# Performance work log

Measured on AMD Instinct MI355X. Metric: run time of the kernel, lower is better.

Reference implementation:

```python
import jax, jax.numpy as jnp
import numpy as np

B, T, WARM, H, FIN, MLPW = 8192, 30, 24, 128, 8, 128
WX = ['clouds','pres','precip','temp','rh','ghi','wind_x','wind_y']
TL = ['hour_sin','hour_cos','year_sin','year_cos','elev_angle','azimuth_sin','azimuth_cos']


def setup_inputs() -> dict:
    key = jax.random.key(0)
    ks = jax.random.split(key, 32)
    d = {}
    for i, n in enumerate(WX + TL):
        d[n] = jax.random.normal(ks[i], (B, T), dtype=jnp.float32)
    d['irradiance_in'] = jax.random.uniform(ks[20], (B, WARM), dtype=jnp.float32)
    s = lambda fan: 1.0 / np.sqrt(fan).astype(np.float32)
    # LSTM params (flax OptimizedLSTMCell math: fused input/hidden kernels, one bias), gate order i,f,g,o
    d['Wi'] = jax.random.normal(ks[21], (FIN, 4 * H), dtype=jnp.float32) * s(FIN)
    d['Wh'] = jax.random.normal(ks[22], (H, 4 * H), dtype=jnp.float32) * s(H)
    d['b'] = jnp.zeros((4 * H,), jnp.float32)
    # output head: MLP(depth=2, width=128) with relu, then Dense(1)
    d['W1'] = jax.random.normal(ks[23], (H, MLPW), dtype=jnp.float32) * s(H)
    d['b1'] = jnp.zeros((MLPW,), jnp.float32)
    d['W2'] = jax.random.normal(ks[24], (MLPW, MLPW), dtype=jnp.float32) * s(MLPW)
    d['b2'] = jnp.zeros((MLPW,), jnp.float32)
    d['Wout'] = jax.random.normal(ks[25], (MLPW, 1), dtype=jnp.float32) * s(MLPW)
    d['bout'] = jnp.zeros((1,), jnp.float32)
    return d


def reference(clouds, pres, precip, temp, rh, ghi, wind_x, wind_y,
              hour_sin, hour_cos, year_sin, year_cos, elev_angle, azimuth_sin, azimuth_cos,
              irradiance_in, Wi, Wh, b, W1, b1, W2, b2, Wout, bout):
    # FLAGS.weather=False path: x is the time/location feature stack [B, T, 7].
    # Weather features are accepted (as in the original dict) but unused.
    x = jnp.stack([hour_sin, hour_cos, year_sin, year_cos, elev_angle, azimuth_sin, azimuth_cos], axis=-1)
    warm_in = jnp.concatenate([x[:, :WARM], irradiance_in[..., None]], axis=-1)  # [B, 24, 8]
    auto_in = x[:, WARM:]                                                        # [B, 6, 7]

    def lstm_step(c, h, inp):
        z = inp @ Wi + h @ Wh + b                    # [B, 4H]
        i, f, g, o = jnp.split(z, 4, axis=-1)
        c2 = jax.nn.sigmoid(f) * c + jax.nn.sigmoid(i) * jnp.tanh(g)
        h2 = jax.nn.sigmoid(o) * jnp.tanh(c2)
        return c2, h2

    def out_mlp(h):
        h = jax.nn.relu(h @ W1 + b1)
        h = jax.nn.relu(h @ W2 + b2)
        return h @ Wout + bout                       # [..., 1]

    c0 = jnp.zeros((x.shape[0], H), x.dtype)
    h0 = jnp.zeros((x.shape[0], H), x.dtype)

    # warmup: teacher-forced LSTM over observed irradiance
    def warm_step(carry, xt):
        c, h = carry
        c, h = lstm_step(c, h, xt)
        return (c, h), h
    (c, h), hs = jax.lax.scan(warm_step, (c0, h0), jnp.swapaxes(warm_in, 0, 1))
    preds_warm = out_mlp(jnp.swapaxes(hs, 0, 1))     # [B, 24, 1]
    last_pred = preds_warm[:, -1]                    # [B, 1]

    def auto_step(carry, xt):
        c, h, p = carry
        c, h = lstm_step(c, h, jnp.concatenate([xt, p], axis=-1))
        p = out_mlp(h)
        return (c, h, p), p
    _, preds_auto = jax.lax.scan(auto_step, (c, h, last_pred), jnp.swapaxes(auto_in, 0, 1))
    preds_auto = jnp.swapaxes(preds_auto, 0, 1)      # [B, 6, 1]

    pred = jnp.concatenate([preds_warm, preds_auto], axis=1)  # [B, 30, 1]
    return jnp.squeeze(pred, axis=2)                 # [B, 30]
```

## Files before the change

### kernel.cpp

```cpp
#include <hip/hip_runtime.h>


#define T_STEPS 30
#define WARM_N  24

typedef _Float16 h8 __attribute__((ext_vector_type(8)));
typedef __attribute__((ext_vector_type(4))) float float4v;

struct FeatPtrs { const float* f[7]; };

#if __has_builtin(__builtin_amdgcn_rcpf)
#define RCP(x) __builtin_amdgcn_rcpf(x)
#else
#define RCP(x) (1.0f/(x))
#endif

__device__ __forceinline__ float sigm(float x){ return RCP(1.0f + __expf(-x)); }
__device__ __forceinline__ float tanh_(float x){ return 1.0f - 2.0f*RCP(1.0f + __expf(2.0f*x)); }

__global__ void pack_weights(const float* __restrict__ Wi, const float* __restrict__ Wh,
                             const float* __restrict__ W1, const float* __restrict__ W2,
                             _Float16* __restrict__ ws)
{
  int idx = blockIdx.x * 256 + threadIdx.x;
  if (idx >= 224 * 512) return;
  int f    = idx >> 9;
  int r    = idx & 511;
  int lane = r >> 3, j = r & 7;
  int kk   = ((lane >> 4) << 3) + j;
  int c16  = lane & 15;
  float v = 0.0f;
  if (f < 160){
    int wt = f / 20, rem = f % 20, g = rem / 5, ks = rem % 5;
    int col = g * 128 + wt * 16 + c16;
    if (ks == 0) v = (kk < 8) ? Wi[kk * 512 + col] : 0.0f;
    else         v = Wh[((ks - 1) * 32 + kk) * 512 + col];
  } else {
    int f2 = f - 160;
    const float* W = (f2 < 32) ? W1 : W2;
    int f3 = f2 & 31;
    int wt = f3 >> 2, ks = f3 & 3;
    v = W[(ks * 32 + kk) * 128 + wt * 16 + c16];
  }
  ws[idx] = (_Float16)v;
}

#define MFMA16 __builtin_amdgcn_mfma_f32_16x16x32_f16

#define INIT_ACC(ACC) \
  _Pragma("unroll") for (int g_ = 0; g_ < 4; ++g_) \
    _Pragma("unroll") for (int r_ = 0; r_ < 4; ++r_) ACC[g_][r_] = bzv[g_];

#define INIT4(V, B) \
  _Pragma("unroll") for (int r_ = 0; r_ < 4; ++r_) V[r_] = (B);

#define ZA(ACC, M1V, XBUF, HOFF, DO1) \
  { h8 ax_ = *(const h8*)&xp[XBUF][(HOFF) + aoff]; \
    _Pragma("unroll") for (int g_ = 0; g_ < 4; ++g_) \
      ACC[g_] = MFMA16(ax_, Bz[g_][0], ACC[g_], 0, 0, 0); } \
  _Pragma("unroll") for (int ks_ = 0; ks_ < 4; ++ks_){ \
    h8 ah_ = *(const h8*)&hp[ks_ * 1280 + (HOFF) + aoff]; \
    _Pragma("unroll") for (int g_ = 0; g_ < 4; ++g_) \
      ACC[g_] = MFMA16(ah_, Bz[g_][1 + ks_], ACC[g_], 0, 0, 0); \
    if (DO1) M1V = MFMA16(ah_, B1f[ks_], M1V, 0, 0, 0); }

#define WRITE_O1(M1V, HOFF) \
  _Pragma("unroll") for (int r_ = 0; r_ < 4; ++r_) \
    o1p[wb + (HOFF) + (kq * 4 + r_) * 40] = (_Float16)fmaxf(M1V[r_], 0.0f);

#define GATES(ACC, CB, HOFF) \
  _Pragma("unroll") for (int r_ = 0; r_ < 4; ++r_){ \
    float zi_ = ACC[0][r_], zf_ = ACC[1][r_], zg_ = ACC[2][r_], zo_ = ACC[3][r_]; \
    float c2_ = sigm(zf_) * cst[(CB) + r_] + sigm(zi_) * tanh_(zg_); \
    cst[(CB) + r_] = c2_; \
    float h2_ = sigm(zo_) * tanh_(c2_); \
    hp[wb + (HOFF) + (kq * 4 + r_) * 40] = (_Float16)h2_; }

#define DO_MLP2(HOFF, ROWB) \
  { float4v m2_; INIT4(m2_, b2v) \
    _Pragma("unroll") for (int ks_ = 0; ks_ < 4; ++ks_){ \
      h8 a_ = *(const h8*)&o1p[ks_ * 1280 + (HOFF) + aoff]; \
      m2_ = MFMA16(a_, B2f[ks_], m2_, 0, 0, 0); } \
    _Pragma("unroll") for (int r_ = 0; r_ < 4; ++r_) \
      o2s[((ROWB) + kq * 4 + r_) * 132 + w * 16 + c16] = fmaxf(m2_[r_], 0.0f); }

#define HEAD_HALF(TLO, RB, STEP) \
  if (t >= (TLO) && t < (TLO) + 128){ \
    int r_ = (RB) + ((t - (TLO)) >> 3), jj_ = t & 7; \
    const float* orow_ = &o2s[r_ * 132 + jj_ * 16]; \
    const float* wrow_ = &WoutS[jj_ * 16]; \
    float s_ = 0.0f; \
    _Pragma("unroll") for (int q_ = 0; q_ < 16; ++q_) s_ += orow_[q_] * wrow_[q_]; \
    s_ += __shfl_down(s_, 4, 8); s_ += __shfl_down(s_, 2, 8); s_ += __shfl_down(s_, 1, 8); \
    if (jj_ == 0){ float pv_ = s_ + bout0; \
      out[(r0 + r_) * T_STEPS + (STEP)] = pv_; pS[r_] = pv_; } }

#define STAGE_WARM(STEP, BUF) \
  if (t < 256){ \
    float v_ = 0.0f; \
    if (fbase) v_ = fbase[STEP]; \
    else if ((STEP) < WARM_N) v_ = ibase[STEP]; \
    xp[BUF][xslot] = (_Float16)v_; }

#define STAGE_TAIL(STEP, BUF) \
  if (t < 256){ \
    float v_ = fbase ? fbase[STEP] : 0.0f; \
    xp[BUF][xslot] = (_Float16)v_; }

__global__ __launch_bounds__(512, 2)
void lstm_mfma(FeatPtrs fp, const float* __restrict__ irr,
               const _Float16* __restrict__ wsb,
               const float* __restrict__ bz, const float* __restrict__ b1,
               const float* __restrict__ b2, const float* __restrict__ Wout,
               const float* __restrict__ bout, float* __restrict__ out)
{
  __shared__ __align__(16) _Float16 xp[2][1280];
  __shared__ __align__(16) _Float16 hp [4 * 1280];
  __shared__ __align__(16) _Float16 o1p[4 * 1280];
  __shared__ __align__(16) float o2s[32 * 132];
  __shared__ float WoutS[128];
  __shared__ float pS[32];

  const int t   = threadIdx.x;
  const int l   = t & 63;
  const int w   = t >> 6;
  const int c16 = l & 15;
  const int kq  = l >> 4;
  const int r0  = blockIdx.x * 32;

  h8 Bz[4][5], B1f[4], B2f[4];
  {
    const h8* f8 = (const h8*)wsb;
#pragma unroll
    for (int g = 0; g < 4; ++g)
#pragma unroll
      for (int ks = 0; ks < 5; ++ks)
        Bz[g][ks] = f8[((w * 4 + g) * 5 + ks) * 64 + l];
#pragma unroll
    for (int ks = 0; ks < 4; ++ks) B1f[ks] = f8[(160 + w * 4 + ks) * 64 + l];
#pragma unroll
    for (int ks = 0; ks < 4; ++ks) B2f[ks] = f8[(192 + w * 4 + ks) * 64 + l];
  }
  float bzv[4], wi7[4];
#pragma unroll
  for (int g = 0; g < 4; ++g){
    bzv[g] = bz[g * 128 + w * 16 + c16];
    wi7[g] = (float)wsb[((w * 4 + g) * 5) * 512 + c16 * 8 + 7];
  }
  const float b1v   = b1[w * 16 + c16];
  const float b2v   = b2[w * 16 + c16];
  const float bout0 = bout[0];
  if (t < 128) WoutS[t] = Wout[t];

  const float* fbase = nullptr;
  const float* ibase = nullptr;
  int xslot = 0;
  if (t < 256){
    int r = t >> 3, j = t & 7;
    if (j < 7) fbase = fp.f[j] + (r0 + r) * T_STEPS;
    else       ibase = irr + (r0 + r) * WARM_N;
    xslot = (r >> 4) * 640 + (r & 15) * 40 + j;
  }

  {
    int* zp = (int*)&xp[0][0];
    for (int i = t; i < 1280; i += 512) zp[i] = 0;
    zp = (int*)hp;
    for (int i = t; i < 2560; i += 512) zp[i] = 0;
  }

  float cst[8];
#pragma unroll
  for (int i = 0; i < 8; ++i) cst[i] = 0.0f;

  const int aoff = c16 * 40 + kq * 8;
  const int wb   = (w >> 1) * 1280 + (w & 1) * 16 + c16;
  __syncthreads();

  if (t < 256){
    float v0 = fbase ? fbase[0] : ibase[0];
    xp[0][xslot] = (_Float16)v0;
  }
  __syncthreads();

  float4v acc0[4], acc1[4];
  float4v m1a, m1b;

  STAGE_WARM(1, 1)
  INIT_ACC(acc0)
  ZA(acc0, m1a, 0, 0, 0)
  __syncthreads();

  INIT_ACC(acc1)
  ZA(acc1, m1b, 0, 640, 0)
  GATES(acc0, 0, 0)
  __syncthreads();

  STAGE_WARM(2, 0)
  INIT_ACC(acc0)
  INIT4(m1a, b1v)
  ZA(acc0, m1a, 1, 0, 1)
  WRITE_O1(m1a, 0)
  GATES(acc1, 4, 640)
  __syncthreads();

  INIT_ACC(acc1)
  INIT4(m1b, b1v)
  ZA(acc1, m1b, 1, 640, 1)
  WRITE_O1(m1b, 640)
  GATES(acc0, 0, 0)
  DO_MLP2(0, 0)
  __syncthreads();

  for (int i = 2; i < 24; ++i){
    const int xbi = i & 1, xbo = (i + 1) & 1;
    STAGE_WARM(i + 1, xbo)
    INIT_ACC(acc0)
    INIT4(m1a, b1v)
    ZA(acc0, m1a, xbi, 0, 1)
    WRITE_O1(m1a, 0)
    GATES(acc1, 4, 640)
    DO_MLP2(640, 16)
    HEAD_HALF(0, 0, i - 2)
    __syncthreads();

    INIT_ACC(acc1)
    INIT4(m1b, b1v)
    ZA(acc1, m1b, xbi, 640, 1)
    WRITE_O1(m1b, 640)
    GATES(acc0, 0, 0)
    DO_MLP2(0, 0)
    HEAD_HALF(128, 16, i - 2)
    __syncthreads();
  }

  GATES(acc1, 4, 640)
  DO_MLP2(640, 16)
  HEAD_HALF(0, 0, 22)
  __syncthreads();
  HEAD_HALF(128, 16, 22)
  __syncthreads();

  for (int s = 24; s < T_STEPS; ++s){
    if (s <= 28){ STAGE_TAIL(s + 1, (s + 1) & 1) }
    float4v acc[4][2];
#pragma unroll
    for (int g = 0; g < 4; ++g)
#pragma unroll
      for (int m = 0; m < 2; ++m)
#pragma unroll
        for (int r = 0; r < 4; ++r) acc[g][m][r] = bzv[g];
    float4v m1[2];
#pragma unroll
    for (int m = 0; m < 2; ++m)
#pragma unroll
      for (int r = 0; r < 4; ++r) m1[m][r] = b1v;
    {
      const _Float16* xb = xp[s & 1];
      h8 a0 = *(const h8*)&xb[aoff];
      h8 a1 = *(const h8*)&xb[640 + aoff];
#pragma unroll
      for (int g = 0; g < 4; ++g){
        acc[g][0] = MFMA16(a0, Bz[g][0], acc[g][0], 0, 0, 0);
        acc[g][1] = MFMA16(a1, Bz[g][0], acc[g][1], 0, 0, 0);
      }
    }
#pragma unroll
    for (int ks = 0; ks < 4; ++ks){
      h8 ah0 = *(const h8*)&hp[ks * 1280 + aoff];
      h8 ah1 = *(const h8*)&hp[ks * 1280 + 640 + aoff];
#pragma unroll
      for (int g = 0; g < 4; ++g){
        acc[g][0] = MFMA16(ah0, Bz[g][1 + ks], acc[g][0], 0, 0, 0);
        acc[g][1] = MFMA16(ah1, Bz[g][1 + ks], acc[g][1], 0, 0, 0);
      }
      m1[0] = MFMA16(ah0, B1f[ks], m1[0], 0, 0, 0);
      m1[1] = MFMA16(ah1, B1f[ks], m1[1], 0, 0, 0);
    }
#pragma unroll
    for (int m = 0; m < 2; ++m)
#pragma unroll
      for (int r = 0; r < 4; ++r)
        o1p[wb + m * 640 + (kq * 4 + r) * 40] = (_Float16)fmaxf(m1[m][r], 0.0f);
    __syncthreads();

    DO_MLP2(0, 0)
    DO_MLP2(640, 16)
    __syncthreads();

    HEAD_HALF(0, 0, s - 1)
    HEAD_HALF(128, 16, s - 1)
    __syncthreads();

#pragma unroll
    for (int m = 0; m < 2; ++m)
#pragma unroll
      for (int r = 0; r < 4; ++r){
        float pv = pS[m * 16 + kq * 4 + r];
#pragma unroll
        for (int g = 0; g < 4; ++g) acc[g][m][r] += pv * wi7[g];
      }
#pragma unroll
    for (int m = 0; m < 2; ++m)
#pragma unroll
      for (int r = 0; r < 4; ++r){
        float zi = acc[0][m][r], zf = acc[1][m][r], zg = acc[2][m][r], zo = acc[3][m][r];
        float c2 = sigm(zf) * cst[m * 4 + r] + sigm(zi) * tanh_(zg);
        cst[m * 4 + r] = c2;
        float h2 = sigm(zo) * tanh_(c2);
        hp[wb + m * 640 + (kq * 4 + r) * 40] = (_Float16)h2;
      }
    __syncthreads();
  }

  {
    float4v m1[2];
#pragma unroll
    for (int m = 0; m < 2; ++m)
#pragma unroll
      for (int r = 0; r < 4; ++r) m1[m][r] = b1v;
#pragma unroll
    for (int ks = 0; ks < 4; ++ks){
      h8 ah0 = *(const h8*)&hp[ks * 1280 + aoff];
      h8 ah1 = *(const h8*)&hp[ks * 1280 + 640 + aoff];
      m1[0] = MFMA16(ah0, B1f[ks], m1[0], 0, 0, 0);
      m1[1] = MFMA16(ah1, B1f[ks], m1[1], 0, 0, 0);
    }
#pragma unroll
    for (int m = 0; m < 2; ++m)
#pragma unroll
      for (int r = 0; r < 4; ++r)
        o1p[wb + m * 640 + (kq * 4 + r) * 40] = (_Float16)fmaxf(m1[m][r], 0.0f);
    __syncthreads();
    DO_MLP2(0, 0)
    DO_MLP2(640, 16)
    __syncthreads();
    HEAD_HALF(0, 0, 29)
    HEAD_HALF(128, 16, 29)
  }
}

extern "C" void kernel_launch(void* const* d_in, const int* in_sizes, int n_in,
                              void* d_out, int out_size, void* d_ws, size_t ws_size,
                              hipStream_t stream)
{
  (void)in_sizes; (void)n_in; (void)out_size; (void)ws_size;
  FeatPtrs fp;
  for (int j = 0; j < 7; ++j) fp.f[j] = (const float*)d_in[8 + j];
  const float* irr  = (const float*)d_in[15];
  const float* Wi   = (const float*)d_in[16];
  const float* Wh   = (const float*)d_in[17];
  const float* bz   = (const float*)d_in[18];
  const float* W1   = (const float*)d_in[19];
  const float* b1   = (const float*)d_in[20];
  const float* W2   = (const float*)d_in[21];
  const float* b2   = (const float*)d_in[22];
  const float* Wout = (const float*)d_in[23];
  const float* bout = (const float*)d_in[24];

  _Float16* ws = (_Float16*)d_ws;
  pack_weights<<<dim3(448), dim3(256), 0, stream>>>(Wi, Wh, W1, W2, ws);
  lstm_mfma<<<dim3(256), dim3(512), 0, stream>>>(
      fp, irr, ws, bz, b1, b2, Wout, bout, (float*)d_out);
}
```

Before: 178.1 us.

## Drop weight-packing pre-kernel and add sched_group_barrier interleaving in warm loop

Removes the separate pack_weights launch and has each thread gather and convert its MFMA B-fragments directly from the fp32 weight matrices at kernel start. This removes one kernel launch and the round trip through the workspace, at the cost of strided scalar global loads in the prologue of every block. It also inserts sched_group_barrier groups (13 VALU, 2 MFMA) before the barriers in the warm loop to interleave MFMA with the gate math.

```diff
diff --git a/kernel.cpp b/kernel.cpp
--- a/kernel.cpp
+++ b/kernel.cpp
@@ -17,33 +17,6 @@
 
 __device__ __forceinline__ float sigm(float x){ return RCP(1.0f + __expf(-x)); }
 __device__ __forceinline__ float tanh_(float x){ return 1.0f - 2.0f*RCP(1.0f + __expf(2.0f*x)); }
-
-__global__ void pack_weights(const float* __restrict__ Wi, const float* __restrict__ Wh,
-                             const float* __restrict__ W1, const float* __restrict__ W2,
-                             _Float16* __restrict__ ws)
-{
-  int idx = blockIdx.x * 256 + threadIdx.x;
-  if (idx >= 224 * 512) return;
-  int f    = idx >> 9;
-  int r    = idx & 511;
-  int lane = r >> 3, j = r & 7;
-  int kk   = ((lane >> 4) << 3) + j;
-  int c16  = lane & 15;
-  float v = 0.0f;
-  if (f < 160){
-    int wt = f / 20, rem = f % 20, g = rem / 5, ks = rem % 5;
-    int col = g * 128 + wt * 16 + c16;
-    if (ks == 0) v = (kk < 8) ? Wi[kk * 512 + col] : 0.0f;
-    else         v = Wh[((ks - 1) * 32 + kk) * 512 + col];
-  } else {
-    int f2 = f - 160;
-    const float* W = (f2 < 32) ? W1 : W2;
-    int f3 = f2 & 31;
-    int wt = f3 >> 2, ks = f3 & 3;
-    v = W[(ks * 32 + kk) * 128 + wt * 16 + c16];
-  }
-  ws[idx] = (_Float16)v;
-}
 
 #define MFMA16 __builtin_amdgcn_mfma_f32_16x16x32_f16
 
@@ -107,10 +80,18 @@
     float v_ = fbase ? fbase[STEP] : 0.0f; \
     xp[BUF][xslot] = (_Float16)v_; }
 
+#define SGB_PAIR \
+  __builtin_amdgcn_sched_group_barrier(0x002, 13, 0); \
+  __builtin_amdgcn_sched_group_barrier(0x008, 2, 0);
+#define SGB_REGION \
+  SGB_PAIR SGB_PAIR SGB_PAIR SGB_PAIR SGB_PAIR SGB_PAIR SGB_PAIR \
+  SGB_PAIR SGB_PAIR SGB_PAIR SGB_PAIR SGB_PAIR SGB_PAIR SGB_PAIR
+
 __global__ __launch_bounds__(512, 2)
 void lstm_mfma(FeatPtrs fp, const float* __restrict__ irr,
-               const _Float16* __restrict__ wsb,
-               const float* __restrict__ bz, const float* __restrict__ b1,
+               const float* __restrict__ Wi, const float* __restrict__ Wh,
+               const float* __restrict__ bz, const float* __restrict__ W1,
+               const float* __restrict__ b1, const float* __restrict__ W2,
                const float* __restrict__ b2, const float* __restrict__ Wout,
                const float* __restrict__ bout, float* __restrict__ out)
 {
@@ -127,28 +108,44 @@
   const int c16 = l & 15;
   const int kq  = l >> 4;
   const int r0  = blockIdx.x * 32;
+  const int colz = w * 16 + c16;
 
   h8 Bz[4][5], B1f[4], B2f[4];
-  {
-    const h8* f8 = (const h8*)wsb;
-#pragma unroll
-    for (int g = 0; g < 4; ++g)
-#pragma unroll
-      for (int ks = 0; ks < 5; ++ks)
-        Bz[g][ks] = f8[((w * 4 + g) * 5 + ks) * 64 + l];
-#pragma unroll
-    for (int ks = 0; ks < 4; ++ks) B1f[ks] = f8[(160 + w * 4 + ks) * 64 + l];
-#pragma unroll
-    for (int ks = 0; ks < 4; ++ks) B2f[ks] = f8[(192 + w * 4 + ks) * 64 + l];
+#pragma unroll
+  for (int g = 0; g < 4; ++g){
+    int col = g * 128 + colz;
+    h8 bx;
+#pragma unroll
+    for (int j = 0; j < 8; ++j)
+      bx[j] = (kq == 0) ? (_Float16)Wi[j * 512 + col] : (_Float16)0.0f;
+    Bz[g][0] = bx;
+#pragma unroll
+    for (int ks = 0; ks < 4; ++ks){
+      h8 bh;
+#pragma unroll
+      for (int j = 0; j < 8; ++j)
+        bh[j] = (_Float16)Wh[(ks * 32 + kq * 8 + j) * 512 + col];
+      Bz[g][1 + ks] = bh;
+    }
+  }
+#pragma unroll
+  for (int ks = 0; ks < 4; ++ks){
+    h8 b1f, b2f;
+#pragma unroll
+    for (int j = 0; j < 8; ++j){
+      b1f[j] = (_Float16)W1[(ks * 32 + kq * 8 + j) * 128 + colz];
+      b2f[j] = (_Float16)W2[(ks * 32 + kq * 8 + j) * 128 + colz];
+    }
+    B1f[ks] = b1f; B2f[ks] = b2f;
   }
   float bzv[4], wi7[4];
 #pragma unroll
   for (int g = 0; g < 4; ++g){
-    bzv[g] = bz[g * 128 + w * 16 + c16];
-    wi7[g] = (float)wsb[((w * 4 + g) * 5) * 512 + c16 * 8 + 7];
-  }
-  const float b1v   = b1[w * 16 + c16];
-  const float b2v   = b2[w * 16 + c16];
+    bzv[g] = bz[g * 128 + colz];
+    wi7[g] = (float)(_Float16)Wi[7 * 512 + g * 128 + colz];
+  }
+  const float b1v   = b1[colz];
+  const float b2v   = b2[colz];
   const float bout0 = bout[0];
   if (t < 128) WoutS[t] = Wout[t];
 
@@ -222,6 +219,7 @@
     GATES(acc1, 4, 640)
     DO_MLP2(640, 16)
     HEAD_HALF(0, 0, i - 2)
+    SGB_REGION
     __syncthreads();
 
     INIT_ACC(acc1)
@@ -231,6 +229,7 @@
     GATES(acc0, 0, 0)
     DO_MLP2(0, 0)
     HEAD_HALF(128, 16, i - 2)
+    SGB_REGION
     __syncthreads();
   }
 
@@ -344,7 +343,7 @@
                               void* d_out, int out_size, void* d_ws, size_t ws_size,
                               hipStream_t stream)
 {
-  (void)in_sizes; (void)n_in; (void)out_size; (void)ws_size;
+  (void)in_sizes; (void)n_in; (void)out_size; (void)d_ws; (void)ws_size;
   FeatPtrs fp;
   for (int j = 0; j < 7; ++j) fp.f[j] = (const float*)d_in[8 + j];
   const float* irr  = (const float*)d_in[15];
@@ -358,8 +357,6 @@
   const float* Wout = (const float*)d_in[23];
   const float* bout = (const float*)d_in[24];
 
-  _Float16* ws = (_Float16*)d_ws;
-  pack_weights<<<dim3(448), dim3(256), 0, stream>>>(Wi, Wh, W1, W2, ws);
   lstm_mfma<<<dim3(256), dim3(512), 0, stream>>>(
-      fp, irr, ws, bz, b1, b2, Wout, bout, (float*)d_out);
+      fp, irr, Wi, Wh, bz, W1, b1, W2, b2, Wout, bout, (float*)d_out);
 }
```

After: 196.7 us. 1.1x slower.
